# Kernel optimization log

Hardware: AMD Instinct MI355X
Metric: run time of the kernel (lower is better)

## Reference

```python
import jax, jax.numpy as jnp
import numpy as np

N_QUBITS = 8
N_LAYERS = 2
FILTERS = 2
K = 2  # kernelsize


def _rx(theta):
    # RX(theta) = [[cos(t/2), -i sin(t/2)], [-i sin(t/2), cos(t/2)]]
    c = jnp.cos(theta / 2)
    s = jnp.sin(theta / 2)
    row0 = jnp.stack([c + 0j, -1j * s])
    row1 = jnp.stack([-1j * s, c + 0j])
    return jnp.stack([row0, row1]).astype(jnp.complex64)


def _apply_1q(state, U, q):
    # state: (2,)*n complex
    state = jnp.moveaxis(state, q, 0)
    state = jnp.tensordot(U, state, axes=[[1], [0]])
    return jnp.moveaxis(state, 0, q)


_CNOT = jnp.array([[1, 0, 0, 0],
                   [0, 1, 0, 0],
                   [0, 0, 0, 1],
                   [0, 0, 1, 0]], dtype=jnp.complex64)


def _apply_cnot(state, c, t):
    n = state.ndim
    state = jnp.moveaxis(state, (c, t), (0, 1))
    shp = state.shape
    state = state.reshape(4, -1)
    state = _CNOT @ state
    state = state.reshape(shp)
    return jnp.moveaxis(state, (0, 1), (c, t))


def _circuit(feat, weights):
    # feat: (K*K,) patch values; weights: (N_LAYERS, N_QUBITS)
    n = N_QUBITS
    state = jnp.zeros((2,) * n, dtype=jnp.complex64).at[(0,) * n].set(1.0)
    # AngleEmbedding (RX) on first K*K wires
    for i in range(K * K):
        state = _apply_1q(state, _rx(feat[i]), i)
    # BasicEntanglerLayers: RX on every wire, then ring of CNOTs
    for l in range(N_LAYERS):
        for q in range(n):
            state = _apply_1q(state, _rx(weights[l, q]), q)
        for q in range(n):
            state = _apply_cnot(state, q, (q + 1) % n)
    probs = jnp.abs(state) ** 2  # (2,)*n real
    z = []
    for q in range(n):
        pq = jnp.moveaxis(probs, q, 0)
        z.append(pq[0].sum() - pq[1].sum())  # expval PauliZ_q
    return jnp.stack(z)  # (n,)


def setup_inputs() -> dict:
    key = jax.random.key(0)
    k1, k2 = jax.random.split(key)
    x = jax.random.normal(k1, (8, 3, 40, 40), dtype=jnp.float32)
    weights = jax.random.normal(k2, (N_LAYERS, N_QUBITS), dtype=jnp.float32)
    return {"x": x, "weights": weights}


def reference(x, weights):
    bs, ch, h, w = x.shape
    h_out = (h - K) // 1 + 1
    w_out = (w - K) // 1 + 1
    # sliding-window patches: (bs, ch, h_out, w_out, K*K)
    patches = jnp.stack(
        [x[:, :, dj:dj + h_out, dk:dk + w_out] for dj in range(K) for dk in range(K)],
        axis=-1,
    )
    feats = patches.reshape(-1, K * K)  # (N, K*K)
    q = jax.vmap(_circuit, in_axes=(0, None))(feats, weights)  # (N, N_QUBITS)
    out = q[:, :FILTERS].reshape(bs, ch, h_out, w_out, FILTERS)
    out = out.mean(axis=1)  # channel-sum then /ch
    out = jnp.moveaxis(out, -1, 1)  # (bs, FILTERS, h_out, w_out)
    return out.astype(jnp.float32)
```

## Files before the change

kernel.cpp:

```cpp
#include <hip/hip_runtime.h>


namespace {

__device__ __forceinline__ float dpp_xor1(float x) {
    return __int_as_float(__builtin_amdgcn_mov_dpp(__float_as_int(x), 0xB1, 0xF, 0xF, true));
}
__device__ __forceinline__ float dpp_xor2(float x) {
    return __int_as_float(__builtin_amdgcn_mov_dpp(__float_as_int(x), 0x4E, 0xF, 0xF, true));
}
__device__ __forceinline__ float dpp_xor8(float x) {
    return __int_as_float(__builtin_amdgcn_mov_dpp(__float_as_int(x), 0x128, 0xF, 0xF, true));
}

template<int M>
__device__ __forceinline__ void rx_local(float (&sr)[16], float (&si)[16], float c, float s) {
#pragma unroll
    for (int r = 0; r < 16; ++r) {
        if (r & M) continue;
        const int a = r, b = r | M;
        float nra = c*sr[a] + s*si[b], nia = c*si[a] - s*sr[b];
        float nrb = c*sr[b] + s*si[a], nib = c*si[b] - s*sr[a];
        sr[a]=nra; si[a]=nia; sr[b]=nrb; si[b]=nib;
    }
}

__device__ __forceinline__ void rx_lane16(float (&sr)[16], float (&si)[16], float c, float s, int mask) {
#pragma unroll
    for (int r = 0; r < 16; ++r) {
        float orr = __shfl_xor(sr[r], mask, 64);
        float oii = __shfl_xor(si[r], mask, 64);
        sr[r] = c*sr[r] + s*oii;
        si[r] = c*si[r] - s*orr;
    }
}

template<int MASK>
__device__ __forceinline__ void rx_lane_dpp(float (&sr)[16], float (&si)[16], float c, float s) {
#pragma unroll
    for (int r = 0; r < 16; ++r) {
        float orr = (MASK == 1) ? dpp_xor1(sr[r]) : (MASK == 2) ? dpp_xor2(sr[r]) : dpp_xor8(sr[r]);
        float oii = (MASK == 1) ? dpp_xor1(si[r]) : (MASK == 2) ? dpp_xor2(si[r]) : dpp_xor8(si[r]);
        sr[r] = c*sr[r] + s*oii;
        si[r] = c*si[r] - s*orr;
    }
}

template<int C, int T>
__device__ __forceinline__ void cnot_ll(float (&sr)[16], float (&si)[16]) {
#pragma unroll
    for (int r = 0; r < 16; ++r) {
        if (!(r & C) || (r & T)) continue;
        const int a = r, b = r ^ T;
        float tr=sr[a], ti=si[a];
        sr[a]=sr[b]; si[a]=si[b];
        sr[b]=tr;    si[b]=ti;
    }
}

__device__ __forceinline__ void entangler(float (&sr)[16], float (&si)[16],
                                          const float* __restrict__ w, int lane) {
    float c, s;
#pragma unroll 1
    for (int l = 0; l < 2; ++l) {
        __sincosf(0.5f*w[l*8+0], &s, &c); rx_local<1>(sr, si, c, s);
        __sincosf(0.5f*w[l*8+1], &s, &c); rx_local<2>(sr, si, c, s);
        __sincosf(0.5f*w[l*8+2], &s, &c); rx_local<4>(sr, si, c, s);
        __sincosf(0.5f*w[l*8+3], &s, &c); rx_local<8>(sr, si, c, s);
        __sincosf(0.5f*w[l*8+4], &s, &c); rx_lane_dpp<1>(sr, si, c, s);
        __sincosf(0.5f*w[l*8+5], &s, &c); rx_lane_dpp<2>(sr, si, c, s);
        __sincosf(0.5f*w[l*8+6], &s, &c); rx_lane16(sr, si, c, s, 4);
        __sincosf(0.5f*w[l*8+7], &s, &c); rx_lane_dpp<8>(sr, si, c, s);

        cnot_ll<1,2>(sr, si);
        cnot_ll<2,4>(sr, si);
        cnot_ll<4,8>(sr, si);
#pragma unroll
        for (int r = 8; r < 16; ++r) {
            sr[r] = dpp_xor1(sr[r]);
            si[r] = dpp_xor1(si[r]);
        }
        {
            const bool ctrl = lane & 1;
#pragma unroll
            for (int r = 0; r < 16; ++r) {
                float orr = dpp_xor2(sr[r]);
                float oii = dpp_xor2(si[r]);
                sr[r] = ctrl ? orr : sr[r];
                si[r] = ctrl ? oii : si[r];
            }
        }
        {
            const bool ctrl = (lane >> 1) & 1;
#pragma unroll
            for (int r = 0; r < 16; ++r) {
                float orr = __shfl_xor(sr[r], 4, 64);
                float oii = __shfl_xor(si[r], 4, 64);
                sr[r] = ctrl ? orr : sr[r];
                si[r] = ctrl ? oii : si[r];
            }
        }
        {
            const bool ctrl = (lane >> 2) & 1;
#pragma unroll
            for (int r = 0; r < 16; ++r) {
                float orr = dpp_xor8(sr[r]);
                float oii = dpp_xor8(si[r]);
                sr[r] = ctrl ? orr : sr[r];
                si[r] = ctrl ? oii : si[r];
            }
        }
        {
            const bool c7 = (lane >> 3) & 1;
#pragma unroll
            for (int r = 0; r < 16; r += 2) {
                float ar = c7 ? sr[r+1] : sr[r];
                float ai = c7 ? si[r+1] : si[r];
                float br = c7 ? sr[r]   : sr[r+1];
                float bi = c7 ? si[r]   : si[r+1];
                sr[r]=ar; si[r]=ai; sr[r+1]=br; si[r+1]=bi;
            }
        }
    }
}

__device__ __forceinline__ int uidx(int n, int g) { return n*16 + g + (n>>4); }

__device__ __forceinline__ void tri_decode(int t, int& rr, int& rp) {
    int r = 0, rem = t;
    while (rem >= 16 - r) { rem -= 16 - r; ++r; }
    rr = r; rp = r + rem;
}

__device__ __forceinline__ int ilv(int bra, int ket) {
    int idx = 0;
#pragma unroll
    for (int k = 0; k < 4; ++k)
        idx |= (((bra>>k)&1) << (2*k+1)) | (((ket>>k)&1) << (2*k));
    return idx;
}

__device__ __forceinline__ void emb_sincos(const float (&f)[12],
                                           float (&vy)[3][4], float (&vz)[3][4]) {
#pragma unroll
    for (int c = 0; c < 3; ++c) {
#pragma unroll
        for (int k = 0; k < 4; ++k) {
            float s, co;
            __sincosf(f[c*4+k], &s, &co);
            vy[c][k] = -s; vz[c][k] = co;
        }
    }
}

}

#define NPIX (8*39*39)
#define BLK  1024
#define PPB  128
#define NBLK ((NPIX + PPB - 1) / PPB)

__global__ __launch_bounds__(1024) void quanv_fused(
    const float* __restrict__ x,
    const float* __restrict__ w,
    float* __restrict__ out)
{
    __shared__ float2 U[16*256 + 16];
    __shared__ float2 XA[2][256];
    __shared__ float2 XB[2][256];
    __shared__ float2 PB[4][2][136];
    __shared__ __align__(16) float Tp[216];

    const int tid  = (int)threadIdx.x;
    const int lane = tid & 63;

    const int gp   = tid - 256;
    const int gpix = (int)blockIdx.x * PPB + (gp & 127);
    const int half = (gp >> 7) & 1;
    const bool is_contract = (tid >= 256) && (tid < 512) && (gpix < NPIX);

    const int pid = (gpix < NPIX) ? gpix : (NPIX - 1);
    const int j  = pid % 39;
    const int t2 = pid / 39;
    const int i  = t2 % 39;
    const int b  = t2 / 39;

    float f[12];
    float vy[3][4], vz[3][4];
    if (tid >= 256 && tid < 512) {
#pragma unroll
        for (int c = 0; c < 3; ++c) {
            const float* xp = x + (((b*3 + c)*40) + i)*40 + j;
            f[c*4+0] = xp[0];  f[c*4+1] = xp[1];
            f[c*4+2] = xp[40]; f[c*4+3] = xp[41];
        }
    }

    if (tid < 256) {
        const int g = (tid >> 6) * 4 + (lane >> 4);
        float sr[16], si[16];
#pragma unroll
        for (int r = 0; r < 16; ++r) {
            sr[r] = (((lane & 15) == 0) && (r == g)) ? 1.f : 0.f;
            si[r] = 0.f;
        }
        entangler(sr, si, w, lane);
#pragma unroll
        for (int r = 0; r < 16; ++r) {
            const int n = ((lane & 15) << 4) | r;
            U[uidx(n, g)] = make_float2(sr[r], si[r]);
        }
    } else if (tid < 512) {
        emb_sincos(f, vy, vz);
    }
    __syncthreads();

    if (tid < 544) {
        const int t = tid >> 2, quarter = tid & 3;
        int rr, rp; tri_decode(t, rr, rp);
        float2 a0={0,0}, a1={0,0}, a2={0,0}, a3={0,0};
        const int n0 = quarter * 64;
        for (int n = n0; n < n0 + 64; n += 4) {
#pragma unroll
            for (int cls = 0; cls < 4; ++cls) {
                const float2 ur = U[uidx(n+cls, rr)];
                const float2 up = U[uidx(n+cls, rp)];
                const float cre = ur.x*up.x + ur.y*up.y;
                const float cim = ur.x*up.y - ur.y*up.x;
                if      (cls==0) { a0.x += cre; a0.y += cim; }
                else if (cls==1) { a1.x += cre; a1.y += cim; }
                else if (cls==2) { a2.x += cre; a2.y += cim; }
                else             { a3.x += cre; a3.y += cim; }
            }
        }
        PB[quarter][0][t] = make_float2((a0.x - a1.x) + (a2.x - a3.x),
                                        (a0.y - a1.y) + (a2.y - a3.y));
        PB[quarter][1][t] = make_float2((a0.x + a1.x) - (a2.x + a3.x),
                                        (a0.y + a1.y) - (a2.y + a3.y));
    }
    __syncthreads();

    if (tid < 136) {
        int rr, rp; tri_decode(tid, rr, rp);
        const int idx  = ilv(rr, rp);
        const int idxT = ilv(rp, rr);
#pragma unroll
        for (int q = 0; q < 2; ++q) {
            float2 m = PB[0][q][tid];
            m.x += PB[1][q][tid].x + PB[2][q][tid].x + PB[3][q][tid].x;
            m.y += PB[1][q][tid].y + PB[2][q][tid].y + PB[3][q][tid].y;
            XA[q][idxT] = make_float2(m.x, -m.y);
            XA[q][idx]  = m;
        }
    }
    __syncthreads();

    float2 (*A)[256] = XA;
    float2 (*B)[256] = XB;
    for (int k = 0; k < 4; ++k) {
        if (tid < 128) {
            const int q = tid >> 6, quad = tid & 63;
            const int st = 1 << (2*k);
            const int ml = st - 1;
            const int base = (quad & ml) | ((quad & ~ml) << 2);
            const float2 i00 = A[q][base],      i01 = A[q][base+st];
            const float2 i10 = A[q][base+2*st], i11 = A[q][base+3*st];
            B[q][base]      = make_float2(0.5f*(i00.x+i11.x), 0.5f*(i00.y+i11.y));
            B[q][base+st]   = make_float2(0.5f*(i01.x+i10.x), 0.5f*(i01.y+i10.y));
            B[q][base+2*st] = make_float2(-0.5f*(i01.y-i10.y), 0.5f*(i01.x-i10.x));
            B[q][base+3*st] = make_float2(0.5f*(i00.x-i11.x), 0.5f*(i00.y-i11.y));
        }
        __syncthreads();
        float2 (*t)[256] = A; A = B; B = t;
    }

    if (tid < 162) {
        const int q = tid / 81, u = tid % 81;
        const int i0 = u % 3, i1 = (u/3) % 3, i2 = (u/9) % 3, i3 = u / 27;
        const int p0 = (i0==0)?0:(i0+1);
        const int p1 = (i1==0)?0:(i1+1);
        const int p2 = (i2==0)?0:(i2+1);
        const int p3 = (i3==0)?0:(i3+1);
        const int idx = p0 | (p1<<2) | (p2<<4) | (p3<<6);
        Tp[q*108 + (u/3)*4 + i0] = A[q][idx].x * (1.f/3.f);
    }
    __syncthreads();

    if (is_contract) {
        float a3[3] = {0.f, 0.f, 0.f};
#pragma unroll
        for (int i3 = 0; i3 < 3; ++i3) {
            float a2[3] = {0.f, 0.f, 0.f};
#pragma unroll
            for (int i2 = 0; i2 < 3; ++i2) {
                float a1[3] = {0.f, 0.f, 0.f};
#pragma unroll
                for (int i1 = 0; i1 < 3; ++i1) {
                    const float4 tv = *reinterpret_cast<const float4*>(
                        &Tp[half*108 + ((i3*3 + i2)*3 + i1)*4]);
#pragma unroll
                    for (int c = 0; c < 3; ++c) {
                        const float s = fmaf(tv.z, vz[c][0], fmaf(tv.y, vy[c][0], tv.x));
                        if      (i1 == 0) a1[c] += s;
                        else if (i1 == 1) a1[c] = fmaf(s, vy[c][1], a1[c]);
                        else              a1[c] = fmaf(s, vz[c][1], a1[c]);
                    }
                }
#pragma unroll
                for (int c = 0; c < 3; ++c) {
                    if      (i2 == 0) a2[c] += a1[c];
                    else if (i2 == 1) a2[c] = fmaf(a1[c], vy[c][2], a2[c]);
                    else              a2[c] = fmaf(a1[c], vz[c][2], a2[c]);
                }
            }
#pragma unroll
            for (int c = 0; c < 3; ++c) {
                if      (i3 == 0) a3[c] += a2[c];
                else if (i3 == 1) a3[c] = fmaf(a2[c], vy[c][3], a3[c]);
                else              a3[c] = fmaf(a2[c], vz[c][3], a3[c]);
            }
        }

        out[((b*2 + half)*39 + i)*39 + j] = a3[0] + a3[1] + a3[2];
    }
}

extern "C" void kernel_launch(void* const* d_in, const int* in_sizes, int n_in,
                              void* d_out, int out_size, void* d_ws, size_t ws_size,
                              hipStream_t stream) {
    const float* x = (const float*)d_in[0];
    const float* w = (const float*)d_in[1];
    float* out = (float*)d_out;

    quanv_fused<<<NBLK, BLK, 0, stream>>>(x, w, out);
}
```

Before: 16.83 us.

## Fuse four Pauli-basis passes into two register passes and shrink block to 576

Replaces the four-stage Pauli-basis transform, which ran 128 threads with a barrier after each stage, with two passes that each apply two stages in registers on a 4x4 tile per thread (32 threads each). This halves the number of block-wide barriers on that serial stretch. Block size and launch bounds drop from 1024 to 576, presumably matching the threads actually used, which may allow more blocks per CU. The cost is less parallelism in the transform and more registers per thread there.

```diff
diff --git a/kernel.cpp b/kernel.cpp
--- a/kernel.cpp
+++ b/kernel.cpp
@@ -140,6 +140,40 @@
     return idx;
 }
 
+__device__ __forceinline__ void pauli4(const float2 i00, const float2 i01,
+                                       const float2 i10, const float2 i11,
+                                       float2& oI, float2& oX, float2& oY, float2& oZ) {
+    oI = make_float2(0.5f*(i00.x+i11.x), 0.5f*(i00.y+i11.y));
+    oX = make_float2(0.5f*(i01.x+i10.x), 0.5f*(i01.y+i10.y));
+    oY = make_float2(-0.5f*(i01.y-i10.y), 0.5f*(i01.x-i10.x));
+    oZ = make_float2(0.5f*(i00.x-i11.x), 0.5f*(i00.y-i11.y));
+}
+
+__device__ __forceinline__ void pauli_pass2(const float2* src, float2* dst,
+                                            int base, int st1, int st2) {
+    float2 v[4][4];
+#pragma unroll
+    for (int a = 0; a < 4; ++a)
+#pragma unroll
+        for (int bq = 0; bq < 4; ++bq)
+            v[a][bq] = src[base + a*st1 + bq*st2];
+    float2 t[4][4];
+#pragma unroll
+    for (int bq = 0; bq < 4; ++bq)
+        pauli4(v[0][bq], v[1][bq], v[2][bq], v[3][bq],
+               t[0][bq], t[1][bq], t[2][bq], t[3][bq]);
+    float2 o[4][4];
+#pragma unroll
+    for (int p1 = 0; p1 < 4; ++p1)
+        pauli4(t[p1][0], t[p1][1], t[p1][2], t[p1][3],
+               o[p1][0], o[p1][1], o[p1][2], o[p1][3]);
+#pragma unroll
+    for (int p1 = 0; p1 < 4; ++p1)
+#pragma unroll
+        for (int p2 = 0; p2 < 4; ++p2)
+            dst[base + p1*st1 + p2*st2] = o[p1][p2];
+}
+
 __device__ __forceinline__ void emb_sincos(const float (&f)[12],
                                            float (&vy)[3][4], float (&vz)[3][4]) {
 #pragma unroll
@@ -156,11 +190,11 @@
 }
 
 #define NPIX (8*39*39)
-#define BLK  1024
+#define BLK  576
 #define PPB  128
 #define NBLK ((NPIX + PPB - 1) / PPB)
 
-__global__ __launch_bounds__(1024) void quanv_fused(
+__global__ __launch_bounds__(576) void quanv_fused(
     const float* __restrict__ x,
     const float* __restrict__ w,
     float* __restrict__ out)
@@ -255,24 +289,16 @@
     }
     __syncthreads();
 
-    float2 (*A)[256] = XA;
-    float2 (*B)[256] = XB;
-    for (int k = 0; k < 4; ++k) {
-        if (tid < 128) {
-            const int q = tid >> 6, quad = tid & 63;
-            const int st = 1 << (2*k);
-            const int ml = st - 1;
-            const int base = (quad & ml) | ((quad & ~ml) << 2);
-            const float2 i00 = A[q][base],      i01 = A[q][base+st];
-            const float2 i10 = A[q][base+2*st], i11 = A[q][base+3*st];
-            B[q][base]      = make_float2(0.5f*(i00.x+i11.x), 0.5f*(i00.y+i11.y));
-            B[q][base+st]   = make_float2(0.5f*(i01.x+i10.x), 0.5f*(i01.y+i10.y));
-            B[q][base+2*st] = make_float2(-0.5f*(i01.y-i10.y), 0.5f*(i01.x-i10.x));
-            B[q][base+3*st] = make_float2(0.5f*(i00.x-i11.x), 0.5f*(i00.y-i11.y));
-        }
-        __syncthreads();
-        float2 (*t)[256] = A; A = B; B = t;
-    }
+    if (tid < 32) {
+        const int q = tid >> 4, pos = tid & 15;
+        pauli_pass2(XA[q], XB[q], pos << 4, 1, 4);
+    }
+    __syncthreads();
+    if (tid < 32) {
+        const int q = tid >> 4, pos = tid & 15;
+        pauli_pass2(XB[q], XA[q], pos, 16, 64);
+    }
+    __syncthreads();
 
     if (tid < 162) {
         const int q = tid / 81, u = tid % 81;
@@ -282,7 +308,7 @@
         const int p2 = (i2==0)?0:(i2+1);
         const int p3 = (i3==0)?0:(i3+1);
         const int idx = p0 | (p1<<2) | (p2<<4) | (p3<<6);
-        Tp[q*108 + (u/3)*4 + i0] = A[q][idx].x * (1.f/3.f);
+        Tp[q*108 + (u/3)*4 + i0] = XA[q][idx].x * (1.f/3.f);
     }
     __syncthreads();
 
```

After: 16.81 us. About the same (-0.1%).
